# Performance work log

Measured on AMD Instinct MI355X. Metric: run time of the kernel, lower is better.

Reference implementation:

```python
import jax, jax.numpy as jnp
import numpy as np

N = 50000   # nodes
E = 800000  # edges (avg degree 16)
D = 128     # input_dim
H = 128     # hidden_dim
OUT = 2     # final GCNConv output dim (hard-coded in module)


def setup_inputs() -> dict:
    key = jax.random.key(0)
    ks = jax.random.split(key, 8)
    x = jax.random.normal(ks[0], (N, D), jnp.float32)
    edge_index = jax.random.randint(ks[1], (2, E), 0, N, dtype=jnp.int32)
    # Glorot-ish init for weights
    W1 = jax.random.normal(ks[2], (D, H), jnp.float32) / np.sqrt(D)
    b1 = jnp.zeros((H,), jnp.float32)
    W2 = jax.random.normal(ks[3], (H, H), jnp.float32) / np.sqrt(H)
    b2 = jnp.zeros((H,), jnp.float32)
    W3 = jax.random.normal(ks[4], (H, OUT), jnp.float32) / np.sqrt(H)
    b3 = jnp.zeros((OUT,), jnp.float32)
    return {"x": x, "edge_index": edge_index,
            "W1": W1, "b1": b1, "W2": W2, "b2": b2, "W3": W3, "b3": b3}


def _gcn_layer(h, W, b, src, dst, norm, n):
    # PyG GCNConv: transform, then normalized sparse aggregation, then bias.
    h = h @ W                                   # [n, out_dim]
    msg = h[src] * norm[:, None]                # gather + edge-normalize
    agg = jax.ops.segment_sum(msg, dst, num_segments=n)  # scatter-add
    return agg + b


def reference(x, edge_index, W1, b1, W2, b2, W3, b3):
    n = x.shape[0]
    loops = jnp.arange(n, dtype=edge_index.dtype)
    src = jnp.concatenate([edge_index[0], loops])  # add self-loops
    dst = jnp.concatenate([edge_index[1], loops])
    # symmetric normalization: D^{-1/2} (A + I) D^{-1/2}
    deg = jax.ops.segment_sum(jnp.ones_like(dst, jnp.float32), dst, num_segments=n)
    dis = jax.lax.rsqrt(deg)                    # deg >= 1 due to self-loops
    norm = dis[src] * dis[dst]                  # [E + n]

    h = jax.nn.relu(_gcn_layer(x, W1, b1, src, dst, norm, n))
    # dropout omitted: eval mode (training=False)
    h = jax.nn.relu(_gcn_layer(h, W2, b2, src, dst, norm, n))
    out = _gcn_layer(h, W3, b3, src, dst, norm, n)
    return out
```

## Files before the change

kernel.cpp:

```cpp
#include <hip/hip_runtime.h>


typedef unsigned short ushort_t;
typedef unsigned int uint_t;

#define NBLK 128
#define BCAP 6144

static __device__ __forceinline__ ushort_t f2bf(float f) {
    uint_t u = __float_as_uint(f);
    u += 0x7FFFu + ((u >> 16) & 1u);
    return (ushort_t)(u >> 16);
}
static __device__ __forceinline__ float bf_lo(uint_t u) {
    return __uint_as_float(u << 16);
}
static __device__ __forceinline__ float bf_hi(uint_t u) {
    return __uint_as_float(u & 0xFFFF0000u);
}

__global__ __launch_bounds__(256) void k_bcount(const int* __restrict__ dst, int E,
                                                int* __restrict__ cntmat, int NB) {
    __shared__ int hist[256];
    int t = threadIdx.x;
    hist[t] = 0;
    __syncthreads();
    int chunk = (E + NBLK - 1) / NBLK;
    int e0 = blockIdx.x * chunk;
    int e1 = min(e0 + chunk, E);
    for (int e = e0 + t; e < e1; e += 256) {
        atomicAdd(&hist[dst[e] >> 8], 1);
    }
    __syncthreads();
    if (t < NB) cntmat[blockIdx.x * NB + t] = hist[t];
}

__global__ __launch_bounds__(256) void k_bscan(int* __restrict__ cntmat,
                                               int* __restrict__ bktbase,
                                               int* __restrict__ rowptr,
                                               int NB, int n, int E) {
    __shared__ int s[256];
    int t = threadIdx.x;
    int acc = 0;
    if (t < NB) {
        for (int r = 0; r < NBLK; r++) {
            int idx = r * NB + t;
            int c = cntmat[idx];
            cntmat[idx] = acc;
            acc += c;
        }
    }
    s[t] = acc;
    __syncthreads();
    for (int off = 1; off < 256; off <<= 1) {
        int u = (t >= off) ? s[t - off] : 0;
        __syncthreads();
        s[t] += u;
        __syncthreads();
    }
    if (t <= NB) bktbase[t] = s[t] - ((t < NB) ? acc : 0);
    if (t == 0) rowptr[n] = E;
}

__global__ __launch_bounds__(256) void k_bfill(const int* __restrict__ src,
                                               const int* __restrict__ dst, int E,
                                               const int* __restrict__ cntmat,
                                               const int* __restrict__ bktbase,
                                               uint_t* __restrict__ bucketed, int NB) {
    __shared__ int runb[256];
    __shared__ int bb[257];
    __shared__ int cur[256];
    int t = threadIdx.x;
    if (t < NB) {
        runb[t] = cntmat[blockIdx.x * NB + t];
        cur[t] = 0;
    }
    if (t < NB + 1) bb[t] = bktbase[t];
    __syncthreads();
    int chunk = (E + NBLK - 1) / NBLK;
    int e0 = blockIdx.x * chunk;
    int e1 = min(e0 + chunk, E);
    for (int e = e0 + t; e < e1; e += 256) {
        int d = dst[e];
        int b = d >> 8;
        int slot = atomicAdd(&cur[b], 1);
        bucketed[bb[b] + runb[b] + slot] = ((uint_t)src[e] << 8) | (uint_t)(d & 255);
    }
}

__global__ __launch_bounds__(256) void k_csort(const uint_t* __restrict__ bucketed,
                                               const int* __restrict__ bktbase,
                                               int* __restrict__ rowptr,
                                               float* __restrict__ dis,
                                               int* __restrict__ csr_src, int n) {
    __shared__ int ncnt[256];
    __shared__ int s[256];
    __shared__ int nofs[256];
    __shared__ int cur[256];
    __shared__ int sorted[BCAP];
    int t = threadIdx.x;
    int b = blockIdx.x;
    int base = bktbase[b];
    int cnt_b = bktbase[b + 1] - base;
    int d0 = b << 8;

    ncnt[t] = 0;
    __syncthreads();
    for (int i = t; i < cnt_b; i += 256) {
        atomicAdd(&ncnt[bucketed[base + i] & 255u], 1);
    }
    __syncthreads();
    int own = ncnt[t];
    s[t] = own;
    __syncthreads();
    for (int off = 1; off < 256; off <<= 1) {
        int u = (t >= off) ? s[t - off] : 0;
        __syncthreads();
        s[t] += u;
        __syncthreads();
    }
    int ex = s[t] - own;
    nofs[t] = ex;
    cur[t] = ex;
    int d = d0 + t;
    if (d < n) {
        rowptr[d] = base + ex;
        dis[d] = rsqrtf((float)(own + 1));
    }
    __syncthreads();
    for (int i = t; i < cnt_b; i += 256) {
        uint_t ent = bucketed[base + i];
        int p = atomicAdd(&cur[ent & 255u], 1);
        if (p < BCAP) sorted[p] = (int)(ent >> 8);
    }
    __syncthreads();
    for (int i = t; i < cnt_b; i += 256) {
        csr_src[base + i] = sorted[i];
    }
}

__global__ __launch_bounds__(256) void k_gemm128(const float* __restrict__ A,
                                                 const float* __restrict__ W,
                                                 ushort_t* __restrict__ C, int n) {
    __shared__ float As[64 * 128];
    __shared__ float Wc[32 * 128];
    int t = threadIdx.x;
    int r0 = blockIdx.x * 64;

    for (int i = t; i < 64 * 128 / 4; i += 256) {
        int gr = r0 + (i >> 5);
        float4 val = (gr < n) ? ((const float4*)A)[(size_t)gr * 32 + (i & 31)]
                              : make_float4(0.f, 0.f, 0.f, 0.f);
        ((float4*)As)[i] = val;
    }

    int c4 = (t & 31) * 4;
    int r8 = (t >> 5) * 8;
    float acc[8][4] = {};

    for (int kc = 0; kc < 4; kc++) {
        __syncthreads();
        for (int i = t; i < 32 * 128 / 4; i += 256) {
            ((float4*)Wc)[i] = ((const float4*)W)[kc * 1024 + i];
        }
        __syncthreads();
#pragma unroll
        for (int kk = 0; kk < 32; kk++) {
            float4 w4 = *(const float4*)&Wc[kk * 128 + c4];
            int k = kc * 32 + kk;
#pragma unroll
            for (int i = 0; i < 8; i++) {
                float a = As[(r8 + i) * 128 + k];
                acc[i][0] += a * w4.x;
                acc[i][1] += a * w4.y;
                acc[i][2] += a * w4.z;
                acc[i][3] += a * w4.w;
            }
        }
    }
#pragma unroll
    for (int i = 0; i < 8; i++) {
        int r = r0 + r8 + i;
        if (r < n) {
            ushort4 o;
            o.x = f2bf(acc[i][0]);
            o.y = f2bf(acc[i][1]);
            o.z = f2bf(acc[i][2]);
            o.w = f2bf(acc[i][3]);
            *(ushort4*)&C[(size_t)r * 128 + c4] = o;
        }
    }
}

__global__ __launch_bounds__(256) void k_agg128(const ushort_t* __restrict__ H,
                                                const int* __restrict__ rowptr,
                                                const int* __restrict__ csr_src,
                                                const float* __restrict__ dis,
                                                const float* __restrict__ bias,
                                                float* __restrict__ O, int n, int do_relu) {
    int wid = threadIdx.x >> 6;
    int lane = threadIdx.x & 63;
    int v = blockIdx.x * 4 + wid;
    if (v >= n) return;

    float dv = dis[v];
    float sw = dv * dv;
    uint_t h2 = ((const uint_t*)(H + (size_t)v * 128))[lane];
    float ax = bf_lo(h2) * sw, ay = bf_hi(h2) * sw;

    int e = rowptr[v], end = rowptr[v + 1];
    for (; e + 4 <= end; e += 4) {
        int s0 = csr_src[e], s1 = csr_src[e + 1], s2 = csr_src[e + 2], s3 = csr_src[e + 3];
        float w0 = dis[s0] * dv, w1 = dis[s1] * dv, w2 = dis[s2] * dv, w3 = dis[s3] * dv;
        uint_t a0 = ((const uint_t*)(H + (size_t)s0 * 128))[lane];
        uint_t a1 = ((const uint_t*)(H + (size_t)s1 * 128))[lane];
        uint_t a2 = ((const uint_t*)(H + (size_t)s2 * 128))[lane];
        uint_t a3 = ((const uint_t*)(H + (size_t)s3 * 128))[lane];
        ax += bf_lo(a0) * w0 + bf_lo(a1) * w1 + bf_lo(a2) * w2 + bf_lo(a3) * w3;
        ay += bf_hi(a0) * w0 + bf_hi(a1) * w1 + bf_hi(a2) * w2 + bf_hi(a3) * w3;
    }
    for (; e < end; e++) {
        int sI = csr_src[e];
        float w = dis[sI] * dv;
        uint_t a = ((const uint_t*)(H + (size_t)sI * 128))[lane];
        ax += bf_lo(a) * w;
        ay += bf_hi(a) * w;
    }

    float2 b2 = ((const float2*)bias)[lane];
    ax += b2.x;
    ay += b2.y;
    if (do_relu) {
        ax = fmaxf(ax, 0.f);
        ay = fmaxf(ay, 0.f);
    }
    ((float2*)(O + (size_t)v * 128))[lane] = make_float2(ax, ay);
}

__global__ __launch_bounds__(256) void k_gemm_out(const float* __restrict__ A,
                                                  const float* __restrict__ W,
                                                  float* __restrict__ T, int n) {
    __shared__ float Wls[256];
    if (threadIdx.x < 256) Wls[threadIdx.x] = W[threadIdx.x];
    __syncthreads();
    int v = blockIdx.x * blockDim.x + threadIdx.x;
    if (v >= n) return;
    const float4* Av = (const float4*)(A + (size_t)v * 128);
    float acc0 = 0.f, acc1 = 0.f;
#pragma unroll
    for (int i = 0; i < 32; i++) {
        float4 a = Av[i];
        int k = i * 4;
        acc0 += a.x * Wls[(k + 0) * 2] + a.y * Wls[(k + 1) * 2] +
                a.z * Wls[(k + 2) * 2] + a.w * Wls[(k + 3) * 2];
        acc1 += a.x * Wls[(k + 0) * 2 + 1] + a.y * Wls[(k + 1) * 2 + 1] +
                a.z * Wls[(k + 2) * 2 + 1] + a.w * Wls[(k + 3) * 2 + 1];
    }
    ((float2*)T)[v] = make_float2(acc0, acc1);
}

__global__ __launch_bounds__(256) void k_agg2(const float* __restrict__ T,
                                              const int* __restrict__ rowptr,
                                              const int* __restrict__ csr_src,
                                              const float* __restrict__ dis,
                                              const float* __restrict__ b3,
                                              float* __restrict__ out, int n) {
    int v = blockIdx.x * blockDim.x + threadIdx.x;
    if (v >= n) return;
    float dv = dis[v];
    float sw = dv * dv;
    float2 tv = ((const float2*)T)[v];
    float a0 = tv.x * sw, a1 = tv.y * sw;
    int end = rowptr[v + 1];
    for (int e = rowptr[v]; e < end; e++) {
        int s = csr_src[e];
        float w = dis[s] * dv;
        float2 hs = ((const float2*)T)[s];
        a0 += hs.x * w;
        a1 += hs.y * w;
    }
    ((float2*)out)[v] = make_float2(a0 + b3[0], a1 + b3[1]);
}

extern "C" void kernel_launch(void* const* d_in, const int* in_sizes, int n_in,
                              void* d_out, int out_size, void* d_ws, size_t ws_size,
                              hipStream_t stream) {
    const float* x  = (const float*)d_in[0];
    const int* edge = (const int*)d_in[1];
    const float* W1 = (const float*)d_in[2];
    const float* b1 = (const float*)d_in[3];
    const float* W2 = (const float*)d_in[4];
    const float* b2 = (const float*)d_in[5];
    const float* W3 = (const float*)d_in[6];
    const float* b3 = (const float*)d_in[7];

    const int n = in_sizes[0] / 128;
    const int E = in_sizes[1] / 2;
    const int NB = (n + 255) >> 8;
    const int* src = edge;
    const int* dst = edge + E;

    char* p = (char*)d_ws;
    auto alloc = [&](size_t bytes) -> void* {
        void* r = (void*)p;
        p += ((bytes + 255) / 256) * 256;
        return r;
    };
    int*      rowptr   = (int*)alloc((size_t)(n + 1) * 4);
    float*    dis      = (float*)alloc((size_t)n * 4);
    int*      cntmat   = (int*)alloc((size_t)NBLK * NB * 4);
    int*      bktbase  = (int*)alloc((size_t)(NB + 1) * 4);
    uint_t*   bucketed = (uint_t*)alloc((size_t)E * 4);
    int*      csr_src  = (int*)alloc((size_t)E * 4);
    float*    t3       = (float*)alloc((size_t)n * 2 * 4);
    ushort_t* Hbf      = (ushort_t*)alloc((size_t)n * 128 * 2);
    float*    Af       = (float*)alloc((size_t)n * 128 * 4);
    (void)ws_size;

    const int nblk = (n + 255) / 256;

    k_bcount<<<NBLK, 256, 0, stream>>>(dst, E, cntmat, NB);
    k_bscan<<<1, 256, 0, stream>>>(cntmat, bktbase, rowptr, NB, n, E);
    k_bfill<<<NBLK, 256, 0, stream>>>(src, dst, E, cntmat, bktbase, bucketed, NB);
    k_csort<<<NB, 256, 0, stream>>>(bucketed, bktbase, rowptr, dis, csr_src, n);

    const int gblk = (n + 63) / 64;
    const int ablk = (n + 3) / 4;

    k_gemm128<<<gblk, 256, 0, stream>>>(x, W1, Hbf, n);
    k_agg128<<<ablk, 256, 0, stream>>>(Hbf, rowptr, csr_src, dis, b1, Af, n, 1);
    k_gemm128<<<gblk, 256, 0, stream>>>(Af, W2, Hbf, n);
    k_agg128<<<ablk, 256, 0, stream>>>(Hbf, rowptr, csr_src, dis, b2, Af, n, 1);
    k_gemm_out<<<nblk, 256, 0, stream>>>(Af, W3, t3, n);
    k_agg2<<<nblk, 256, 0, stream>>>(t3, rowptr, csr_src, dis, b3, (float*)d_out, n);
}
```

Before: 301.0 us.

## Enlarge GEMM tile to 128 rows with 8x8 register blocking and vector loads

```diff
diff --git a/kernel.cpp b/kernel.cpp
--- a/kernel.cpp
+++ b/kernel.cpp
@@ -95,7 +95,6 @@
                                                int* __restrict__ csr_src, int n) {
     __shared__ int ncnt[256];
     __shared__ int s[256];
-    __shared__ int nofs[256];
     __shared__ int cur[256];
     __shared__ int sorted[BCAP];
     int t = threadIdx.x;
@@ -120,7 +119,6 @@
         __syncthreads();
     }
     int ex = s[t] - own;
-    nofs[t] = ex;
     cur[t] = ex;
     int d = d0 + t;
     if (d < n) {
@@ -142,39 +140,55 @@
 __global__ __launch_bounds__(256) void k_gemm128(const float* __restrict__ A,
                                                  const float* __restrict__ W,
                                                  ushort_t* __restrict__ C, int n) {
-    __shared__ float As[64 * 128];
+    __shared__ float As[128 * 128];
     __shared__ float Wc[32 * 128];
     int t = threadIdx.x;
-    int r0 = blockIdx.x * 64;
-
-    for (int i = t; i < 64 * 128 / 4; i += 256) {
+    int r0 = blockIdx.x * 128;
+
+    for (int i = t; i < 128 * 32; i += 256) {
         int gr = r0 + (i >> 5);
         float4 val = (gr < n) ? ((const float4*)A)[(size_t)gr * 32 + (i & 31)]
                               : make_float4(0.f, 0.f, 0.f, 0.f);
         ((float4*)As)[i] = val;
     }
 
-    int c4 = (t & 31) * 4;
-    int r8 = (t >> 5) * 8;
-    float acc[8][4] = {};
+    int c8 = (t & 15) * 8;
+    int r8 = (t >> 4) * 8;
+    float acc[8][8] = {};
 
     for (int kc = 0; kc < 4; kc++) {
         __syncthreads();
-        for (int i = t; i < 32 * 128 / 4; i += 256) {
+        for (int i = t; i < 32 * 32; i += 256) {
             ((float4*)Wc)[i] = ((const float4*)W)[kc * 1024 + i];
         }
         __syncthreads();
 #pragma unroll
-        for (int kk = 0; kk < 32; kk++) {
-            float4 w4 = *(const float4*)&Wc[kk * 128 + c4];
-            int k = kc * 32 + kk;
+        for (int k4 = 0; k4 < 32; k4 += 4) {
+            float4 a[8];
 #pragma unroll
             for (int i = 0; i < 8; i++) {
-                float a = As[(r8 + i) * 128 + k];
-                acc[i][0] += a * w4.x;
-                acc[i][1] += a * w4.y;
-                acc[i][2] += a * w4.z;
-                acc[i][3] += a * w4.w;
+                a[i] = *(const float4*)&As[(r8 + i) * 128 + kc * 32 + k4];
+            }
+            float4 w[4][2];
+#pragma unroll
+            for (int kk = 0; kk < 4; kk++) {
+                w[kk][0] = *(const float4*)&Wc[(k4 + kk) * 128 + c8];
+                w[kk][1] = *(const float4*)&Wc[(k4 + kk) * 128 + c8 + 4];
+            }
+#pragma unroll
+            for (int i = 0; i < 8; i++) {
+                float av[4] = {a[i].x, a[i].y, a[i].z, a[i].w};
+#pragma unroll
+                for (int kk = 0; kk < 4; kk++) {
+                    acc[i][0] += av[kk] * w[kk][0].x;
+                    acc[i][1] += av[kk] * w[kk][0].y;
+                    acc[i][2] += av[kk] * w[kk][0].z;
+                    acc[i][3] += av[kk] * w[kk][0].w;
+                    acc[i][4] += av[kk] * w[kk][1].x;
+                    acc[i][5] += av[kk] * w[kk][1].y;
+                    acc[i][6] += av[kk] * w[kk][1].z;
+                    acc[i][7] += av[kk] * w[kk][1].w;
+                }
             }
         }
     }
@@ -182,12 +196,13 @@
     for (int i = 0; i < 8; i++) {
         int r = r0 + r8 + i;
         if (r < n) {
-            ushort4 o;
-            o.x = f2bf(acc[i][0]);
-            o.y = f2bf(acc[i][1]);
-            o.z = f2bf(acc[i][2]);
-            o.w = f2bf(acc[i][3]);
-            *(ushort4*)&C[(size_t)r * 128 + c4] = o;
+            ushort4 o0, o1;
+            o0.x = f2bf(acc[i][0]); o0.y = f2bf(acc[i][1]);
+            o0.z = f2bf(acc[i][2]); o0.w = f2bf(acc[i][3]);
+            o1.x = f2bf(acc[i][4]); o1.y = f2bf(acc[i][5]);
+            o1.z = f2bf(acc[i][6]); o1.w = f2bf(acc[i][7]);
+            *(ushort4*)&C[(size_t)r * 128 + c8] = o0;
+            *(ushort4*)&C[(size_t)r * 128 + c8 + 4] = o1;
         }
     }
 }
@@ -324,7 +339,7 @@
     k_bfill<<<NBLK, 256, 0, stream>>>(src, dst, E, cntmat, bktbase, bucketed, NB);
     k_csort<<<NB, 256, 0, stream>>>(bucketed, bktbase, rowptr, dis, csr_src, n);
 
-    const int gblk = (n + 63) / 64;
+    const int gblk = (n + 127) / 128;
     const int ablk = (n + 3) / 4;
 
     k_gemm128<<<gblk, 256, 0, stream>>>(x, W1, Hbf, n);
```

Result: slower. 327.4 us (+8.8%).
